# Kernel tuning notes

Measured on AMD Instinct MI355X. Metric: run time of the kernel, lower is better.

The kernel has to match this reference:

```python
import jax, jax.numpy as jnp
import numpy as np

RATIO = 0.12
# Per output channel (after shuffle [4,5,6,7,0,1,2,3] applied to the first entry of each
# selectable_directions group): (pos_x, pos_y, neg_x, neg_y) offsets into the 3x3 stencil.
# conv2d with a +1/-1 sparse kernel == padded[pos] - padded[neg] neighbor difference.
OFFSETS = [
    (1, 0, 2, 2),  # old filter 4: dirs [9,4]
    (0, 2, 1, 0),  # old filter 5: dirs [4,3]
    (2, 1, 0, 2),  # old filter 6: dirs [3,8]
    (0, 0, 2, 1),  # old filter 7: dirs [8,1]
    (1, 2, 1, 1),  # old filter 0: dirs [5,6]
    (0, 1, 1, 1),  # old filter 1: dirs [5,2]
    (0, 2, 1, 1),  # old filter 2: dirs [5,3]
    (0, 0, 1, 1),  # old filter 3: dirs [5,1]
]


def setup_inputs() -> dict:
    key = jax.random.key(0)
    img = jax.random.uniform(key, (16, 3, 512, 512), dtype=jnp.float32)
    return {"img": img}


def reference(img):
    B, C, H, W = img.shape
    # channel max -> [B,1,H,W]
    img_v = jnp.max(img, axis=1, keepdims=True)
    # replicate pad by 1 on each spatial side -> [B,1,H+2,W+2]
    padded = jnp.pad(img_v, ((0, 0), (0, 0), (1, 1), (1, 1)), mode='edge')
    # per-image dynamic range -> [1,B,1,1,1] (matches unsqueeze(0) in torch code)
    rng = (jnp.max(img_v, axis=(2, 3), keepdims=True)
           - jnp.min(img_v, axis=(2, 3), keepdims=True))[None]
    # sparse +1/-1 3x3 conv as 8 neighbor differences -> [8,B,H,W]
    diffs = jnp.stack(
        [padded[:, 0, px:px + H, py:py + W] - padded[:, 0, nx:nx + H, ny:ny + W]
         for (px, py, nx, ny) in OFFSETS],
        axis=0,
    )
    pos = jnp.maximum(diffs, 0.0)   # all_img_v * (all_img_v >= 0)
    neg = jnp.maximum(-diffs, 0.0)  # -all_img_v * (all_img_v < 0)
    out = jnp.stack([pos, neg], axis=2)  # [8,B,2,H,W]
    return (out >= rng * RATIO).astype(jnp.float32)
```

## Files before the change

kernel.cpp:

```cpp
#include <hip/hip_runtime.h>
#include <cstdint>
#include <cstddef>

typedef float f32x4 __attribute__((ext_vector_type(4)));

constexpr int BB = 16, CC = 3, HH = 512, WW = 512;
constexpr int HW = HH * WW;
constexpr float RATIO = 0.12f;
constexpr int TR = 8;
constexpr int TILES = HH / TR;


__global__ __launch_bounds__(256) void k1_minmax(
        const float* __restrict__ img, float* __restrict__ pmin,
        float* __restrict__ pmax) {
    int t    = blockIdx.x * 256 + threadIdx.x;
    int off4 = t << 2;
    int b    = off4 / HW;
    int off  = off4 - b * HW;
    const float* base = img + (size_t)b * CC * HW + off;
    f32x4 c0 = *(const f32x4*)(base);
    f32x4 c1 = *(const f32x4*)(base + HW);
    f32x4 c2 = *(const f32x4*)(base + 2 * HW);
    f32x4 v;
    v.x = fmaxf(fmaxf(c0.x, c1.x), c2.x);
    v.y = fmaxf(fmaxf(c0.y, c1.y), c2.y);
    v.z = fmaxf(fmaxf(c0.z, c1.z), c2.z);
    v.w = fmaxf(fmaxf(c0.w, c1.w), c2.w);

    float mn = fminf(fminf(v.x, v.y), fminf(v.z, v.w));
    float mx = fmaxf(fmaxf(v.x, v.y), fmaxf(v.z, v.w));
    #pragma unroll
    for (int s = 32; s > 0; s >>= 1) {
        mn = fminf(mn, __shfl_xor(mn, s, 64));
        mx = fmaxf(mx, __shfl_xor(mx, s, 64));
    }
    __shared__ float smn[4], smx[4];
    int wave = threadIdx.x >> 6;
    if ((threadIdx.x & 63) == 0) { smn[wave] = mn; smx[wave] = mx; }
    __syncthreads();
    if (threadIdx.x == 0) {
        pmin[blockIdx.x] = fminf(fminf(smn[0], smn[1]), fminf(smn[2], smn[3]));
        pmax[blockIdx.x] = fmaxf(fmaxf(smx[0], smx[1]), fmaxf(smx[2], smx[3]));
    }
}

__global__ __launch_bounds__(256, 8) void k2_edges(
        const float* __restrict__ img, const float* __restrict__ pmin,
        const float* __restrict__ pmax, float* __restrict__ out) {
    int bid = blockIdx.x;
    int x   = bid & 7;
    int m   = bid >> 3;
    int f   = m & 7;
    int g   = ((m >> 3) << 3) + x;
    int b    = g >> 6;
    int tile = g & 63;
    int t    = threadIdx.x;

    __shared__ float ld[(TR + 2) * WW];

    {
        float mlo = pmin[(b << 8) + t];
        float mhi = pmax[(b << 8) + t];
        #pragma unroll
        for (int s = 32; s > 0; s >>= 1) {
            mlo = fminf(mlo, __shfl_xor(mlo, s, 64));
            mhi = fmaxf(mhi, __shfl_xor(mhi, s, 64));
        }
        if ((t & 63) == 0) { ld[t >> 6] = mlo; ld[4 + (t >> 6)] = mhi; }
    }
    __syncthreads();
    float thr = (fmaxf(fmaxf(ld[4], ld[5]), fmaxf(ld[6], ld[7]))
               - fminf(fminf(ld[0], ld[1]), fminf(ld[2], ld[3]))) * RATIO;
    __syncthreads();

    int tile0 = tile * TR;
    const float* ib = img + (size_t)b * CC * HW;
    #pragma unroll
    for (int s = 0; s < 5; ++s) {
        int v  = t + (s << 8);
        int vr = v >> 7;
        int vc = (v & 127) << 2;
        int g2 = min(max(tile0 - 1 + vr, 0), HH - 1);
        const float* rb = ib + (size_t)g2 * WW + vc;
        f32x4 a0 = *(const f32x4*)(rb);
        f32x4 a1 = *(const f32x4*)(rb + HW);
        f32x4 a2 = *(const f32x4*)(rb + 2 * HW);
        f32x4 q;
        q.x = fmaxf(fmaxf(a0.x, a1.x), a2.x);
        q.y = fmaxf(fmaxf(a0.y, a1.y), a2.y);
        q.z = fmaxf(fmaxf(a0.z, a1.z), a2.z);
        q.w = fmaxf(fmaxf(a0.w, a1.w), a2.w);
        *(f32x4*)&ld[vr * WW + vc] = q;
    }
    __syncthreads();

    int c  = (t & 127) << 2;
    int cl = max(c - 1, 0), cr = min(c + 4, WW - 1);
    int rb2 = t >> 7;
    size_t planep = (size_t)((f * BB + b) * 2) * HW;
    float* outp = out + planep;
    float* outn = out + planep + HW;

    #pragma unroll
    for (int j = 0; j < 4; ++j) {
        int orow = (j << 1) + rb2;
        const float* T = &ld[orow * WW];
        const float* M = &ld[(orow + 1) * WW];
        const float* P = &ld[(orow + 2) * WW];
        float vt[6], vm[6], vp[6];
        { f32x4 q = *(const f32x4*)(T + c);
          vt[0] = T[cl]; vt[1] = q.x; vt[2] = q.y; vt[3] = q.z; vt[4] = q.w; vt[5] = T[cr]; }
        { f32x4 q = *(const f32x4*)(M + c);
          vm[0] = M[cl]; vm[1] = q.x; vm[2] = q.y; vm[3] = q.z; vm[4] = q.w; vm[5] = M[cr]; }
        { f32x4 q = *(const f32x4*)(P + c);
          vp[0] = P[cl]; vp[1] = q.x; vp[2] = q.y; vp[3] = q.z; vp[4] = q.w; vp[5] = P[cr]; }

        float d0, d1, d2, d3;
        switch (f) {
            case 0: d0 = vm[0]-vp[2]; d1 = vm[1]-vp[3]; d2 = vm[2]-vp[4]; d3 = vm[3]-vp[5]; break;
            case 1: d0 = vt[2]-vm[0]; d1 = vt[3]-vm[1]; d2 = vt[4]-vm[2]; d3 = vt[5]-vm[3]; break;
            case 2: d0 = vp[1]-vt[2]; d1 = vp[2]-vt[3]; d2 = vp[3]-vt[4]; d3 = vp[4]-vt[5]; break;
            case 3: d0 = vt[0]-vp[1]; d1 = vt[1]-vp[2]; d2 = vt[2]-vp[3]; d3 = vt[3]-vp[4]; break;
            case 4: d0 = vm[2]-vm[1]; d1 = vm[3]-vm[2]; d2 = vm[4]-vm[3]; d3 = vm[5]-vm[4]; break;
            case 5: d0 = vt[1]-vm[1]; d1 = vt[2]-vm[2]; d2 = vt[3]-vm[3]; d3 = vt[4]-vm[4]; break;
            case 6: d0 = vt[2]-vm[1]; d1 = vt[3]-vm[2]; d2 = vt[4]-vm[3]; d3 = vt[5]-vm[4]; break;
            default:d0 = vt[0]-vm[1]; d1 = vt[1]-vm[2]; d2 = vt[2]-vm[3]; d3 = vt[3]-vm[4]; break;
        }
        f32x4 qp, qn;
        qp.x = (fmaxf(d0, 0.f) >= thr) ? 1.f : 0.f;
        qp.y = (fmaxf(d1, 0.f) >= thr) ? 1.f : 0.f;
        qp.z = (fmaxf(d2, 0.f) >= thr) ? 1.f : 0.f;
        qp.w = (fmaxf(d3, 0.f) >= thr) ? 1.f : 0.f;
        qn.x = (fmaxf(-d0, 0.f) >= thr) ? 1.f : 0.f;
        qn.y = (fmaxf(-d1, 0.f) >= thr) ? 1.f : 0.f;
        qn.z = (fmaxf(-d2, 0.f) >= thr) ? 1.f : 0.f;
        qn.w = (fmaxf(-d3, 0.f) >= thr) ? 1.f : 0.f;

        size_t po = (size_t)(tile0 + orow) * WW + c;
        *(f32x4*)(outp + po) = qp;
        *(f32x4*)(outn + po) = qn;
    }
}

extern "C" void kernel_launch(void* const* d_in, const int* in_sizes, int n_in,
                              void* d_out, int out_size, void* d_ws, size_t ws_size,
                              hipStream_t stream) {
    const float* img = (const float*)d_in[0];
    float* out  = (float*)d_out;
    float* pmin = (float*)d_ws;
    float* pmax = (float*)((char*)d_ws + 16384);

    k1_minmax<<<4096, 256, 0, stream>>>(img, pmin, pmax);
    k2_edges<<<8 * BB * TILES, 256, 0, stream>>>(img, pmin, pmax, out);
}
```

Baseline: 68.20 us.

## Double edge-kernel tile height and load halo rows into registers

Raises the row tile from 8 to 16, so each block writes twice as many output rows and the halo re-read overhead per tile shrinks. The two halo rows are no longer staged in shared memory. Threads 0-127 and 128-255 each load one halo row, plus its edge columns, straight into registers, and use it for the first and last stencil rows. Shared memory per block grows and the grid halves, which may cut occupancy and parallelism. The 8 filter blocks per tile still each reload the image independently.

```diff
diff --git a/kernel.cpp b/kernel.cpp
--- a/kernel.cpp
+++ b/kernel.cpp
@@ -7,7 +7,7 @@
 constexpr int BB = 16, CC = 3, HH = 512, WW = 512;
 constexpr int HW = HH * WW;
 constexpr float RATIO = 0.12f;
-constexpr int TR = 8;
+constexpr int TR = 16;
 constexpr int TILES = HH / TR;
 
 
@@ -53,11 +53,31 @@
     int m   = bid >> 3;
     int f   = m & 7;
     int g   = ((m >> 3) << 3) + x;
-    int b    = g >> 6;
-    int tile = g & 63;
+    int b    = g >> 5;
+    int tile = g & 31;
     int t    = threadIdx.x;
+    int tile0 = tile * TR;
 
-    __shared__ float ld[(TR + 2) * WW];
+    __shared__ float ld[TR * WW];
+
+    const float* ib = img + (size_t)b * CC * HW;
+
+    int hc  = (t & 127) << 2;
+    int hcl = max(hc - 1, 0), hcr = min(hc + 4, WW - 1);
+    int hrow = (t < 128) ? max(tile0 - 1, 0) : min(tile0 + TR, HH - 1);
+    const float* hb = ib + (size_t)hrow * WW;
+    float hal[6];
+    {
+        f32x4 a0 = *(const f32x4*)(hb + hc);
+        f32x4 a1 = *(const f32x4*)(hb + HW + hc);
+        f32x4 a2 = *(const f32x4*)(hb + 2 * HW + hc);
+        hal[1] = fmaxf(fmaxf(a0.x, a1.x), a2.x);
+        hal[2] = fmaxf(fmaxf(a0.y, a1.y), a2.y);
+        hal[3] = fmaxf(fmaxf(a0.z, a1.z), a2.z);
+        hal[4] = fmaxf(fmaxf(a0.w, a1.w), a2.w);
+        hal[0] = fmaxf(fmaxf(hb[hcl], hb[HW + hcl]), hb[2 * HW + hcl]);
+        hal[5] = fmaxf(fmaxf(hb[hcr], hb[HW + hcr]), hb[2 * HW + hcr]);
+    }
 
     {
         float mlo = pmin[(b << 8) + t];
@@ -74,15 +94,12 @@
                - fminf(fminf(ld[0], ld[1]), fminf(ld[2], ld[3]))) * RATIO;
     __syncthreads();
 
-    int tile0 = tile * TR;
-    const float* ib = img + (size_t)b * CC * HW;
     #pragma unroll
-    for (int s = 0; s < 5; ++s) {
+    for (int s = 0; s < 8; ++s) {
         int v  = t + (s << 8);
         int vr = v >> 7;
         int vc = (v & 127) << 2;
-        int g2 = min(max(tile0 - 1 + vr, 0), HH - 1);
-        const float* rb = ib + (size_t)g2 * WW + vc;
+        const float* rb = ib + (size_t)(tile0 + vr) * WW + vc;
         f32x4 a0 = *(const f32x4*)(rb);
         f32x4 a1 = *(const f32x4*)(rb + HW);
         f32x4 a2 = *(const f32x4*)(rb + 2 * HW);
@@ -95,26 +112,36 @@
     }
     __syncthreads();
 
-    int c  = (t & 127) << 2;
-    int cl = max(c - 1, 0), cr = min(c + 4, WW - 1);
+    int c  = hc;
+    int cl = hcl, cr = hcr;
     int rb2 = t >> 7;
     size_t planep = (size_t)((f * BB + b) * 2) * HW;
     float* outp = out + planep;
-    float* outn = out + planep + HW;
+    float* outn = outp + HW;
 
     #pragma unroll
-    for (int j = 0; j < 4; ++j) {
+    for (int j = 0; j < 8; ++j) {
         int orow = (j << 1) + rb2;
-        const float* T = &ld[orow * WW];
-        const float* M = &ld[(orow + 1) * WW];
-        const float* P = &ld[(orow + 2) * WW];
+        const float* T = &ld[max(orow - 1, 0) * WW];
+        const float* M = &ld[orow * WW];
+        const float* P = &ld[min(orow + 1, TR - 1) * WW];
         float vt[6], vm[6], vp[6];
-        { f32x4 q = *(const f32x4*)(T + c);
-          vt[0] = T[cl]; vt[1] = q.x; vt[2] = q.y; vt[3] = q.z; vt[4] = q.w; vt[5] = T[cr]; }
+        if (j == 0 && t < 128) {
+            #pragma unroll
+            for (int q2 = 0; q2 < 6; ++q2) vt[q2] = hal[q2];
+        } else {
+            f32x4 q = *(const f32x4*)(T + c);
+            vt[0] = T[cl]; vt[1] = q.x; vt[2] = q.y; vt[3] = q.z; vt[4] = q.w; vt[5] = T[cr];
+        }
         { f32x4 q = *(const f32x4*)(M + c);
           vm[0] = M[cl]; vm[1] = q.x; vm[2] = q.y; vm[3] = q.z; vm[4] = q.w; vm[5] = M[cr]; }
-        { f32x4 q = *(const f32x4*)(P + c);
-          vp[0] = P[cl]; vp[1] = q.x; vp[2] = q.y; vp[3] = q.z; vp[4] = q.w; vp[5] = P[cr]; }
+        if (j == 7 && t >= 128) {
+            #pragma unroll
+            for (int q2 = 0; q2 < 6; ++q2) vp[q2] = hal[q2];
+        } else {
+            f32x4 q = *(const f32x4*)(P + c);
+            vp[0] = P[cl]; vp[1] = q.x; vp[2] = q.y; vp[3] = q.z; vp[4] = q.w; vp[5] = P[cr];
+        }
 
         float d0, d1, d2, d3;
         switch (f) {
```

After: 66.75 us. 2.1% less time.
